# Kernel optimization log

Hardware: AMD Instinct MI355X
Metric: run time of the kernel (lower is better)

## Reference

```python
import jax, jax.numpy as jnp
import numpy as np

# DeformConv hyperparameters (from init_kwargs)
KH, KW = 3, 3
STRIDE, PAD, DIL = 1, 1, 1
GROUPS, DG = 1, 1  # groups=1, deformable_groups=1
B, C, H, W = 4, 64, 128, 128
O = 64
HO = (H + 2 * PAD - (DIL * (KH - 1) + 1)) // STRIDE + 1  # 128
WO = (W + 2 * PAD - (DIL * (KW - 1) + 1)) // STRIDE + 1  # 128


def setup_inputs() -> dict:
    key = jax.random.key(0)
    k1, k2, k3, k4 = jax.random.split(key, 4)
    x = jax.random.normal(k1, (B, C, H, W), dtype=jnp.float32)
    # offset channels: dg * K * 2, ordered (y, x) per kernel tap (DCNv1 CUDA layout)
    offset = jax.random.normal(k2, (B, 2 * DG * KH * KW, HO, WO), dtype=jnp.float32)
    fan_in = C * KH * KW
    weight = jax.random.normal(k3, (O, C // GROUPS, KH, KW), dtype=jnp.float32) / np.sqrt(fan_in)
    bias = jax.random.normal(k4, (O,), dtype=jnp.float32) * 0.01
    return {"x": x, "offset": offset, "weight": weight, "bias": bias}


def _deform_sample(x, offset):
    """Bilinear-sample x at deformed kernel tap locations.
    Returns [B, C, K, HO, WO] where K = KH*KW."""
    K = KH * KW
    Cg = C // DG
    # offset -> [B, DG, K, 2, HO, WO]; channel layout: dg*2*K, pairs (y, x)
    off = offset.reshape(B, DG, K, 2, HO, WO)
    off_y, off_x = off[:, :, :, 0], off[:, :, :, 1]  # [B, DG, K, HO, WO]

    ki = (jnp.arange(K) // KW).astype(jnp.float32)  # kernel row
    kj = (jnp.arange(K) % KW).astype(jnp.float32)   # kernel col
    base_h = (jnp.arange(HO) * STRIDE - PAD).astype(jnp.float32)
    base_w = (jnp.arange(WO) * STRIDE - PAD).astype(jnp.float32)

    # sampling positions [B, DG, K, HO, WO]
    py = off_y + (ki * DIL)[None, None, :, None, None] + base_h[None, None, None, :, None]
    px = off_x + (kj * DIL)[None, None, :, None, None] + base_w[None, None, None, None, :]

    y0f = jnp.floor(py)
    x0f = jnp.floor(px)
    ly = py - y0f
    lx = px - x0f
    hy = 1.0 - ly
    hx = 1.0 - lx
    y0 = y0f.astype(jnp.int32)
    x0 = x0f.astype(jnp.int32)
    y1 = y0 + 1
    x1 = x0 + 1

    flat = x.reshape(B, DG, Cg, H * W)

    def gather(yi, xi, wgt):
        valid = (yi >= 0) & (yi < H) & (xi >= 0) & (xi < W)
        idx = jnp.clip(yi, 0, H - 1) * W + jnp.clip(xi, 0, W - 1)
        idx = idx.reshape(B, DG, 1, K * HO * WO)
        v = jnp.take_along_axis(flat, idx, axis=-1).reshape(B, DG, Cg, K, HO, WO)
        return v * (wgt * valid.astype(wgt.dtype))[:, :, None]

    val = (gather(y0, x0, hy * hx) + gather(y0, x1, hy * lx)
           + gather(y1, x0, ly * hx) + gather(y1, x1, ly * lx))
    return val.reshape(B, C, K, HO, WO)


def reference(x, offset, weight, bias):
    sampled = _deform_sample(x, offset)              # [B, C, K, HO, WO]
    w = weight.reshape(O, C, KH * KW)                # groups = 1
    out = jnp.einsum('bckhw,ock->bohw', sampled, w)  # im2col + GEMM
    return out + bias[None, :, None, None]
```

## Files before the change

### kernel.cpp

```cpp
#include <hip/hip_runtime.h>
#include <hip/hip_fp16.h>


#define B_  4
#define C_  64
#define H_  128
#define W_  128
#define O_  64
#define HO_ 128
#define WO_ 128
#define NCHUNK 8
#define NGW 12
#define NT_ 32
#define NROW 2
#define NCOL 64
#define NTASK (9 * NCOL)
#define SG  10
#define SBUF (SG * NCOL * 8)
#define TR  14
#define TC  44
#define TSLOTS (TR * TC)
#define TBUF (TSLOTS * 8)

typedef _Float16 half8 __attribute__((ext_vector_type(8)));
typedef __attribute__((ext_vector_type(4))) float f32x4;
typedef __attribute__((ext_vector_type(16))) float f32x16;

union H8 { float4 v; __half2 h2[4]; half8 v8; };

__global__ __launch_bounds__(256)
void prep(const float* __restrict__ x, const float* __restrict__ w,
          __half* __restrict__ xt, __half* __restrict__ wt) {
    const int tid = threadIdx.x;
    if (blockIdx.x < 2048) {
        int t = blockIdx.x * 256 + tid;
        int xc = t & 127;
        int y  = (t >> 7) & 127;
        int ch = (t >> 14) & 7;
        int b  = t >> 17;
        const float* xp = x + (((size_t)(b * C_ + ch * 8) * H_) + y) * W_ + xc;
        union { __half h[8]; float4 v; } pk;
#pragma unroll
        for (int e = 0; e < 8; ++e) pk.h[e] = __float2half_rn(xp[e * H_ * W_]);
        *(float4*)(xt + (size_t)t * 8) = pk.v;
    } else {
        int t = (blockIdx.x - 2048) * 256 + tid;
        if (t >= NCHUNK * NGW * O_) return;
        int o  = t & 63;
        int g  = (t >> 6) % NGW;
        int ch = (t >> 6) / NGW;
        union { __half h[8]; float4 v; } pk;
#pragma unroll
        for (int e = 0; e < 8; ++e)
            pk.h[e] = (g < 9) ? __float2half_rn(w[(o * C_ + ch * 8 + e) * 9 + g])
                              : __half(0.0f);
        *(float4*)(wt + (size_t)t * 8) = pk.v;
    }
}

__global__ __launch_bounds__(256, 4)
void dcn_mfma(const __half* __restrict__ xt, const float* __restrict__ off,
              const __half* __restrict__ wt, const float* __restrict__ bias,
              float* __restrict__ out) {
    __shared__ __align__(16) _Float16 sS[2 * SBUF];
    __shared__ __align__(16) _Float16 sT[2 * TBUF];

    const int tid = threadIdx.x;
    const int bid = blockIdx.x;
    const int w4  = bid & 3;
    const int hp  = (bid >> 2) & 63;
    const int b   = bid >> 8;
    const int ho  = hp << 1;
    const int woB = w4 * NT_;
    const int yb  = ho - 6;
    const int xb  = woB - 6;

    int a0_[3], a1_[3], nf_[3];
    __half2 ua2_[3], ub2_[3], va2_[3], vb2_[3];
#pragma unroll
    for (int r = 0; r < 3; ++r) {
        bool act = (r < 2) || ((tid & 3) == 0);
        if (act) {
            int task = (r < 2) ? (tid + r * 256) : (512 + (tid >> 2));
            int k  = task >> 6;
            int n  = task & 63;
            int wo = (n & 31) + woB;
            int hr = ho + (n >> 5);
            int ki = k / 3, kj = k - 3 * ki;
            float oy = off[(((b * 18) + 2 * k    ) * HO_ + hr) * WO_ + wo];
            float ox = off[(((b * 18) + 2 * k + 1) * HO_ + hr) * WO_ + wo];
            float py = (float)(hr - 1 + ki) + oy;
            float px = (float)(wo - 1 + kj) + ox;
            float y0f = floorf(py), x0f = floorf(px);
            int   y0 = (int)y0f,   x0 = (int)x0f;
            float ly = py - y0f,   lx = px - x0f;
            float hy = 1.f - ly,   hx = 1.f - lx;
            int y1 = y0 + 1, x1 = x0 + 1;
            float vy0 = (y0 >= 0 && y0 < H_) ? 1.f : 0.f;
            float vy1 = (y1 >= 0 && y1 < H_) ? 1.f : 0.f;
            float vx0 = (x0 >= 0 && x0 < W_) ? 1.f : 0.f;
            float vx1 = (x1 >= 0 && x1 < W_) ? 1.f : 0.f;
            int cy0 = min(max(y0, 0), H_ - 1), cy1 = min(max(y1, 0), H_ - 1);
            int ax  = min(max(x0, 0), W_ - 2);
            int cx0 = min(max(x0, 0), W_ - 1), cx1 = min(max(x1, 0), W_ - 1);
            float w00 = hy * hx * vy0 * vx0;
            float w01 = hy * lx * vy0 * vx1;
            float w10 = ly * hx * vy1 * vx0;
            float w11 = ly * lx * vy1 * vx1;
            float s0 = (cx0 != ax) ? 1.f : 0.f;
            float s1 = (cx1 != ax) ? 1.f : 0.f;
            int t0 = cy0 - yb, t1 = cy1 - yb, txx = ax - xb;
            int fb = ((unsigned)t0  > (TR - 1)) |
                     ((unsigned)t1  > (TR - 1)) |
                     ((unsigned)txx > (TC - 2));
            nf_[r] = !fb;
            a0_[r] = fb ? (cy0 * W_ + ax) : (t0 * TC + txx);
            a1_[r] = fb ? (cy1 * W_ + ax) : (t1 * TC + txx);
            ua2_[r] = __float2half2_rn(w00 * (1.f - s0) + w01 * (1.f - s1));
            ub2_[r] = __float2half2_rn(w00 * s0 + w01 * s1);
            va2_[r] = __float2half2_rn(w10 * (1.f - s0) + w11 * (1.f - s1));
            vb2_[r] = __float2half2_rn(w10 * s0 + w11 * s1);
        }
    }

    int gofs[3];
#pragma unroll
    for (int j = 0; j < 3; ++j) {
        int s  = tid + j * 256;
        int sc = (s < TSLOTS) ? s : (TSLOTS - 1);
        int rr = sc / TC, cc = sc - rr * TC;
        int yc = min(max(yb + rr, 0), H_ - 1);
        int xc = min(max(xb + cc, 0), W_ - 1);
        gofs[j] = yc * W_ + xc;
    }

    ((unsigned int*)&sS[9 * NCOL * 8])[tid]        = 0u;
    ((unsigned int*)&sS[SBUF + 9 * NCOL * 8])[tid] = 0u;

    float4 pf0, pf1, pf2;
    auto issue = [&](int ch) {
        const float4* xc = (const float4*)(xt + ((size_t)(b * NCHUNK + ch)) * (H_ * W_ * 8));
        pf0 = xc[gofs[0]];
        pf1 = xc[gofs[1]];
        if (tid < TSLOTS - 512) pf2 = xc[gofs[2]];
    };
    auto tile_write = [&](int parity) {
        float4* tw = (float4*)(sT + parity * TBUF);
        tw[tid]       = pf0;
        tw[tid + 256] = pf1;
        if (tid < TSLOTS - 512) tw[tid + 512] = pf2;
    };

    auto sample = [&](int ch) {
        _Float16* buf = sS + (ch & 1) * SBUF;
        const float4* xcg = (const float4*)(xt + ((size_t)(b * NCHUNK + ch)) * (H_ * W_ * 8));
        const float4* tl  = (const float4*)(sT + (ch & 1) * TBUF);
#pragma unroll
        for (int r = 0; r < 3; ++r) {
            bool act = (r < 2) || ((tid & 3) == 0);
            if (act) {
                int task = (r < 2) ? (tid + r * 256) : (512 + (tid >> 2));
                int k = task >> 6;
                int n = task & 63;
                int a0 = a0_[r], a1 = a1_[r];
                H8 q00, q01, q10, q11;
                if (nf_[r]) {
                    q00.v = tl[a0];  q01.v = tl[a0 + 1];
                    q10.v = tl[a1];  q11.v = tl[a1 + 1];
                } else {
                    q00.v = xcg[a0]; q01.v = xcg[a0 + 1];
                    q10.v = xcg[a1]; q11.v = xcg[a1 + 1];
                }
                H8 s;
#pragma unroll
                for (int j = 0; j < 4; ++j) {
                    __half2 t0 = __hmul2(ua2_[r], q00.h2[j]);
                    t0 = __hfma2(ub2_[r], q01.h2[j], t0);
                    t0 = __hfma2(va2_[r], q10.h2[j], t0);
                    t0 = __hfma2(vb2_[r], q11.h2[j], t0);
                    s.h2[j] = t0;
                }
                *(half8*)&buf[(k * NCOL + n) * 8] = s.v8;
            }
        }
    };

    const int lane = tid & 63;
    const int wv   = tid >> 6;
    const int ow   = wv & 1;
    const int nw   = wv >> 1;
    const int h2k  = lane >> 5;
    const int l31  = lane & 31;

    f32x16 acc = {0.f, 0.f, 0.f, 0.f, 0.f, 0.f, 0.f, 0.f,
                  0.f, 0.f, 0.f, 0.f, 0.f, 0.f, 0.f, 0.f};

    auto mfma_chunk = [&](int ch) {
        const __half*   wc  = wt + (size_t)(ch * NGW) * O_ * 8;
        const _Float16* buf = sS + (ch & 1) * SBUF;
#pragma unroll
        for (int ks = 0; ks < 6; ++ks) {
            int g  = 2 * ks + h2k;
            int gb = (g < 9) ? g : 9;
            half8 bfr = *(const half8*)&buf[(gb * NCOL + nw * 32 + l31) * 8];
            half8 afr = *(const half8*)(wc + (size_t)(g * O_ + ow * 32 + l31) * 8);
            acc = __builtin_amdgcn_mfma_f32_32x32x16_f16(afr, bfr, acc, 0, 0, 0);
        }
    };

    issue(0);
    tile_write(0);
    for (int ch = 0; ch < NCHUNK; ++ch) {
        __syncthreads();
        if (ch + 1 < NCHUNK) issue(ch + 1);
        sample(ch);
        if (ch > 0) mfma_chunk(ch - 1);
        if (ch + 1 < NCHUNK) tile_write((ch + 1) & 1);
    }
    __syncthreads();
    mfma_chunk(NCHUNK - 1);

    {
        int wo = woB + l31;
        size_t base = (((size_t)b * O_) * HO_ + ho + nw) * WO_ + wo;
#pragma unroll
        for (int rg = 0; rg < 16; ++rg) {
            int o = ow * 32 + (rg & 3) + 8 * (rg >> 2) + 4 * h2k;
            out[base + (size_t)o * HO_ * WO_] = acc[rg] + bias[o];
        }
    }
}

extern "C" void kernel_launch(void* const* d_in, const int* in_sizes, int n_in,
                              void* d_out, int out_size, void* d_ws, size_t ws_size,
                              hipStream_t stream) {
    const float* x    = (const float*)d_in[0];
    const float* off  = (const float*)d_in[1];
    const float* w    = (const float*)d_in[2];
    const float* bias = (const float*)d_in[3];
    float* out = (float*)d_out;

    __half* wt = (__half*)d_ws;
    __half* xt = (__half*)((char*)d_ws + 262144);

    hipLaunchKernelGGL(prep, dim3(2048 + 24), dim3(256), 0, stream, x, w, xt, wt);
    hipLaunchKernelGGL(dcn_mfma, dim3(B_ * (HO_ / NROW) * (WO_ / NT_)), dim3(256), 0, stream,
                       xt, off, wt, bias, out);
}
```

Before: 98.41 us.

## Fuse x fp16 transpose into DCN kernel, read NCHW fp32 directly

Removes the separate pass that converted x into a channel-interleaved fp16 buffer. The main kernel now loads fp32 x from NCHW, eight scalar loads per slot, and converts to half when staging the shared tile and in the out-of-tile fallback path. The third task round moves from every fourth thread to the last wave, so the extra work sits in one wavefront instead of causing divergence in all of them. This saves a full read and write of x plus one launch, but each tile load now issues strided scalar reads with more registers held, and the fallback gathers become much more expensive.

```diff
diff --git a/kernel.cpp b/kernel.cpp
--- a/kernel.cpp
+++ b/kernel.cpp
@@ -21,6 +21,7 @@
 #define TC  44
 #define TSLOTS (TR * TC)
 #define TBUF (TSLOTS * 8)
+#define HW_ (H_ * W_)
 
 typedef _Float16 half8 __attribute__((ext_vector_type(8)));
 typedef __attribute__((ext_vector_type(4))) float f32x4;
@@ -29,37 +30,22 @@
 union H8 { float4 v; __half2 h2[4]; half8 v8; };
 
 __global__ __launch_bounds__(256)
-void prep(const float* __restrict__ x, const float* __restrict__ w,
-          __half* __restrict__ xt, __half* __restrict__ wt) {
-    const int tid = threadIdx.x;
-    if (blockIdx.x < 2048) {
-        int t = blockIdx.x * 256 + tid;
-        int xc = t & 127;
-        int y  = (t >> 7) & 127;
-        int ch = (t >> 14) & 7;
-        int b  = t >> 17;
-        const float* xp = x + (((size_t)(b * C_ + ch * 8) * H_) + y) * W_ + xc;
-        union { __half h[8]; float4 v; } pk;
-#pragma unroll
-        for (int e = 0; e < 8; ++e) pk.h[e] = __float2half_rn(xp[e * H_ * W_]);
-        *(float4*)(xt + (size_t)t * 8) = pk.v;
-    } else {
-        int t = (blockIdx.x - 2048) * 256 + tid;
-        if (t >= NCHUNK * NGW * O_) return;
-        int o  = t & 63;
-        int g  = (t >> 6) % NGW;
-        int ch = (t >> 6) / NGW;
-        union { __half h[8]; float4 v; } pk;
-#pragma unroll
-        for (int e = 0; e < 8; ++e)
-            pk.h[e] = (g < 9) ? __float2half_rn(w[(o * C_ + ch * 8 + e) * 9 + g])
-                              : __half(0.0f);
-        *(float4*)(wt + (size_t)t * 8) = pk.v;
-    }
+void prep_wt(const float* __restrict__ w, __half* __restrict__ wt) {
+    int t = blockIdx.x * 256 + threadIdx.x;
+    if (t >= NCHUNK * NGW * O_) return;
+    int o  = t & 63;
+    int g  = (t >> 6) % NGW;
+    int ch = (t >> 6) / NGW;
+    union { __half h[8]; float4 v; } pk;
+#pragma unroll
+    for (int e = 0; e < 8; ++e)
+        pk.h[e] = (g < 9) ? __float2half_rn(w[(o * C_ + ch * 8 + e) * 9 + g])
+                          : __half(0.0f);
+    *(float4*)(wt + (size_t)t * 8) = pk.v;
 }
 
 __global__ __launch_bounds__(256, 4)
-void dcn_mfma(const __half* __restrict__ xt, const float* __restrict__ off,
+void dcn_mfma(const float* __restrict__ x, const float* __restrict__ off,
               const __half* __restrict__ wt, const float* __restrict__ bias,
               float* __restrict__ out) {
     __shared__ __align__(16) _Float16 sS[2 * SBUF];
@@ -75,13 +61,15 @@
     const int yb  = ho - 6;
     const int xb  = woB - 6;
 
+    const float* xb_ = x + (size_t)b * C_ * HW_;
+
     int a0_[3], a1_[3], nf_[3];
     __half2 ua2_[3], ub2_[3], va2_[3], vb2_[3];
 #pragma unroll
     for (int r = 0; r < 3; ++r) {
-        bool act = (r < 2) || ((tid & 3) == 0);
+        bool act = (r < 2) || (tid >= 192);
         if (act) {
-            int task = (r < 2) ? (tid + r * 256) : (512 + (tid >> 2));
+            int task = (r < 2) ? (tid + r * 256) : (512 + (tid & 63));
             int k  = task >> 6;
             int n  = task & 63;
             int wo = (n & 31) + woB;
@@ -137,29 +125,41 @@
     ((unsigned int*)&sS[9 * NCOL * 8])[tid]        = 0u;
     ((unsigned int*)&sS[SBUF + 9 * NCOL * 8])[tid] = 0u;
 
-    float4 pf0, pf1, pf2;
+    float pfv[3][8];
     auto issue = [&](int ch) {
-        const float4* xc = (const float4*)(xt + ((size_t)(b * NCHUNK + ch)) * (H_ * W_ * 8));
-        pf0 = xc[gofs[0]];
-        pf1 = xc[gofs[1]];
-        if (tid < TSLOTS - 512) pf2 = xc[gofs[2]];
+        const float* xc = xb_ + (size_t)(ch * 8) * HW_;
+#pragma unroll
+        for (int j = 0; j < 3; ++j) {
+            if (j < 2 || tid < TSLOTS - 512) {
+#pragma unroll
+                for (int e = 0; e < 8; ++e)
+                    pfv[j][e] = xc[(size_t)e * HW_ + gofs[j]];
+            }
+        }
     };
     auto tile_write = [&](int parity) {
         float4* tw = (float4*)(sT + parity * TBUF);
-        tw[tid]       = pf0;
-        tw[tid + 256] = pf1;
-        if (tid < TSLOTS - 512) tw[tid + 512] = pf2;
+#pragma unroll
+        for (int j = 0; j < 3; ++j) {
+            if (j < 2 || tid < TSLOTS - 512) {
+                H8 pk;
+#pragma unroll
+                for (int jj = 0; jj < 4; ++jj)
+                    pk.h2[jj] = __floats2half2_rn(pfv[j][2 * jj], pfv[j][2 * jj + 1]);
+                tw[tid + j * 256] = pk.v;
+            }
+        }
     };
 
     auto sample = [&](int ch) {
         _Float16* buf = sS + (ch & 1) * SBUF;
-        const float4* xcg = (const float4*)(xt + ((size_t)(b * NCHUNK + ch)) * (H_ * W_ * 8));
-        const float4* tl  = (const float4*)(sT + (ch & 1) * TBUF);
+        const float* xcg = xb_ + (size_t)(ch * 8) * HW_;
+        const float4* tl = (const float4*)(sT + (ch & 1) * TBUF);
 #pragma unroll
         for (int r = 0; r < 3; ++r) {
-            bool act = (r < 2) || ((tid & 3) == 0);
+            bool act = (r < 2) || (tid >= 192);
             if (act) {
-                int task = (r < 2) ? (tid + r * 256) : (512 + (tid >> 2));
+                int task = (r < 2) ? (tid + r * 256) : (512 + (tid & 63));
                 int k = task >> 6;
                 int n = task & 63;
                 int a0 = a0_[r], a1 = a1_[r];
@@ -168,8 +168,18 @@
                     q00.v = tl[a0];  q01.v = tl[a0 + 1];
                     q10.v = tl[a1];  q11.v = tl[a1 + 1];
                 } else {
-                    q00.v = xcg[a0]; q01.v = xcg[a0 + 1];
-                    q10.v = xcg[a1]; q11.v = xcg[a1 + 1];
+#pragma unroll
+                    for (int jj = 0; jj < 4; ++jj) {
+                        int e0 = 2 * jj, e1 = 2 * jj + 1;
+                        q00.h2[jj] = __floats2half2_rn(xcg[(size_t)e0 * HW_ + a0],
+                                                       xcg[(size_t)e1 * HW_ + a0]);
+                        q01.h2[jj] = __floats2half2_rn(xcg[(size_t)e0 * HW_ + a0 + 1],
+                                                       xcg[(size_t)e1 * HW_ + a0 + 1]);
+                        q10.h2[jj] = __floats2half2_rn(xcg[(size_t)e0 * HW_ + a1],
+                                                       xcg[(size_t)e1 * HW_ + a1]);
+                        q11.h2[jj] = __floats2half2_rn(xcg[(size_t)e0 * HW_ + a1 + 1],
+                                                       xcg[(size_t)e1 * HW_ + a1 + 1]);
+                    }
                 }
                 H8 s;
 #pragma unroll
@@ -241,9 +251,8 @@
     float* out = (float*)d_out;
 
     __half* wt = (__half*)d_ws;
-    __half* xt = (__half*)((char*)d_ws + 262144);
-
-    hipLaunchKernelGGL(prep, dim3(2048 + 24), dim3(256), 0, stream, x, w, xt, wt);
+
+    hipLaunchKernelGGL(prep_wt, dim3(24), dim3(256), 0, stream, w, wt);
     hipLaunchKernelGGL(dcn_mfma, dim3(B_ * (HO_ / NROW) * (WO_ / NT_)), dim3(256), 0, stream,
-                       xt, off, wt, bias, out);
+                       x, off, wt, bias, out);
 }
```

Result: slower. 106.1 us (+7.8%).

## Feed bilinear samples directly into 16x16x32 MFMA registers, dropping shared staging

Applied to the files above, without the earlier changes.

Sampled values are no longer written to a shared-memory im2col buffer and read back for a 32x32 MFMA. Each wave now computes its own sampled B-fragment in registers and feeds it straight into four 16x16x32 MFMAs, one per 16-output tile. The halo tile grows to 16x48 so the slot count matches the 768 threads' loads exactly, which removes the predicated load. This drops the LDS round trip and the separate sample/MFMA pipeline stage. In exchange, weight fragments are reloaded per wave, the pipeline depth shrinks, and some lanes do dummy work for the padded taps.

```diff
diff --git a/kernel.cpp b/kernel.cpp
--- a/kernel.cpp
+++ b/kernel.cpp
@@ -13,18 +13,14 @@
 #define NGW 12
 #define NT_ 32
 #define NROW 2
-#define NCOL 64
-#define NTASK (9 * NCOL)
-#define SG  10
-#define SBUF (SG * NCOL * 8)
-#define TR  14
-#define TC  44
+#define TR  16
+#define TC  48
 #define TSLOTS (TR * TC)
 #define TBUF (TSLOTS * 8)
+#define HW_ (H_ * W_)
 
 typedef _Float16 half8 __attribute__((ext_vector_type(8)));
 typedef __attribute__((ext_vector_type(4))) float f32x4;
-typedef __attribute__((ext_vector_type(16))) float f32x16;
 
 union H8 { float4 v; __half2 h2[4]; half8 v8; };
 
@@ -62,7 +58,6 @@
 void dcn_mfma(const __half* __restrict__ xt, const float* __restrict__ off,
               const __half* __restrict__ wt, const float* __restrict__ bias,
               float* __restrict__ out) {
-    __shared__ __align__(16) _Float16 sS[2 * SBUF];
     __shared__ __align__(16) _Float16 sT[2 * TBUF];
 
     const int tid = threadIdx.x;
@@ -73,22 +68,25 @@
     const int ho  = hp << 1;
     const int woB = w4 * NT_;
     const int yb  = ho - 6;
-    const int xb  = woB - 6;
+    const int xb  = woB - 8;
+
+    const int lane = tid & 63;
+    const int wv   = tid >> 6;
+    const int quad = lane >> 4;
+    const int l15  = lane & 15;
+    const int n    = wv * 16 + l15;
+    const int hr   = ho + (n >> 5);
+    const int wo   = woB + (n & 31);
 
     int a0_[3], a1_[3], nf_[3];
     __half2 ua2_[3], ub2_[3], va2_[3], vb2_[3];
 #pragma unroll
-    for (int r = 0; r < 3; ++r) {
-        bool act = (r < 2) || ((tid & 3) == 0);
-        if (act) {
-            int task = (r < 2) ? (tid + r * 256) : (512 + (tid >> 2));
-            int k  = task >> 6;
-            int n  = task & 63;
-            int wo = (n & 31) + woB;
-            int hr = ho + (n >> 5);
-            int ki = k / 3, kj = k - 3 * ki;
-            float oy = off[(((b * 18) + 2 * k    ) * HO_ + hr) * WO_ + wo];
-            float ox = off[(((b * 18) + 2 * k + 1) * HO_ + hr) * WO_ + wo];
+    for (int ks = 0; ks < 3; ++ks) {
+        int g = ks * 4 + quad;
+        if (g < 9) {
+            int ki = g / 3, kj = g - 3 * ki;
+            float oy = off[(((b * 18) + 2 * g    ) * HO_ + hr) * WO_ + wo];
+            float ox = off[(((b * 18) + 2 * g + 1) * HO_ + hr) * WO_ + wo];
             float py = (float)(hr - 1 + ki) + oy;
             float px = (float)(wo - 1 + kj) + ox;
             float y0f = floorf(py), x0f = floorf(px);
@@ -113,13 +111,16 @@
             int fb = ((unsigned)t0  > (TR - 1)) |
                      ((unsigned)t1  > (TR - 1)) |
                      ((unsigned)txx > (TC - 2));
-            nf_[r] = !fb;
-            a0_[r] = fb ? (cy0 * W_ + ax) : (t0 * TC + txx);
-            a1_[r] = fb ? (cy1 * W_ + ax) : (t1 * TC + txx);
-            ua2_[r] = __float2half2_rn(w00 * (1.f - s0) + w01 * (1.f - s1));
-            ub2_[r] = __float2half2_rn(w00 * s0 + w01 * s1);
-            va2_[r] = __float2half2_rn(w10 * (1.f - s0) + w11 * (1.f - s1));
-            vb2_[r] = __float2half2_rn(w10 * s0 + w11 * s1);
+            nf_[ks] = !fb;
+            a0_[ks] = fb ? (cy0 * W_ + ax) : (t0 * TC + txx);
+            a1_[ks] = fb ? (cy1 * W_ + ax) : (t1 * TC + txx);
+            ua2_[ks] = __float2half2_rn(w00 * (1.f - s0) + w01 * (1.f - s1));
+            ub2_[ks] = __float2half2_rn(w00 * s0 + w01 * s1);
+            va2_[ks] = __float2half2_rn(w10 * (1.f - s0) + w11 * (1.f - s1));
+            vb2_[ks] = __float2half2_rn(w10 * s0 + w11 * s1);
+        } else {
+            nf_[ks] = 1; a0_[ks] = 0; a1_[ks] = 0;
+            ua2_[ks] = ub2_[ks] = va2_[ks] = vb2_[ks] = __float2half2_rn(0.f);
         }
     }
 
@@ -127,84 +128,61 @@
 #pragma unroll
     for (int j = 0; j < 3; ++j) {
         int s  = tid + j * 256;
-        int sc = (s < TSLOTS) ? s : (TSLOTS - 1);
-        int rr = sc / TC, cc = sc - rr * TC;
+        int rr = s / TC, cc = s - rr * TC;
         int yc = min(max(yb + rr, 0), H_ - 1);
         int xc = min(max(xb + cc, 0), W_ - 1);
         gofs[j] = yc * W_ + xc;
     }
 
-    ((unsigned int*)&sS[9 * NCOL * 8])[tid]        = 0u;
-    ((unsigned int*)&sS[SBUF + 9 * NCOL * 8])[tid] = 0u;
-
     float4 pf0, pf1, pf2;
     auto issue = [&](int ch) {
-        const float4* xc = (const float4*)(xt + ((size_t)(b * NCHUNK + ch)) * (H_ * W_ * 8));
+        const float4* xc = (const float4*)(xt + ((size_t)(b * NCHUNK + ch)) * (HW_ * 8));
         pf0 = xc[gofs[0]];
         pf1 = xc[gofs[1]];
-        if (tid < TSLOTS - 512) pf2 = xc[gofs[2]];
+        pf2 = xc[gofs[2]];
     };
     auto tile_write = [&](int parity) {
         float4* tw = (float4*)(sT + parity * TBUF);
         tw[tid]       = pf0;
         tw[tid + 256] = pf1;
-        if (tid < TSLOTS - 512) tw[tid + 512] = pf2;
+        tw[tid + 512] = pf2;
     };
 
-    auto sample = [&](int ch) {
-        _Float16* buf = sS + (ch & 1) * SBUF;
-        const float4* xcg = (const float4*)(xt + ((size_t)(b * NCHUNK + ch)) * (H_ * W_ * 8));
+    f32x4 acc[4];
+#pragma unroll
+    for (int ot = 0; ot < 4; ++ot) acc[ot] = (f32x4){0.f, 0.f, 0.f, 0.f};
+
+    auto compute = [&](int ch) {
         const float4* tl  = (const float4*)(sT + (ch & 1) * TBUF);
-#pragma unroll
-        for (int r = 0; r < 3; ++r) {
-            bool act = (r < 2) || ((tid & 3) == 0);
-            if (act) {
-                int task = (r < 2) ? (tid + r * 256) : (512 + (tid >> 2));
-                int k = task >> 6;
-                int n = task & 63;
-                int a0 = a0_[r], a1 = a1_[r];
-                H8 q00, q01, q10, q11;
-                if (nf_[r]) {
-                    q00.v = tl[a0];  q01.v = tl[a0 + 1];
-                    q10.v = tl[a1];  q11.v = tl[a1 + 1];
-                } else {
-                    q00.v = xcg[a0]; q01.v = xcg[a0 + 1];
-                    q10.v = xcg[a1]; q11.v = xcg[a1 + 1];
-                }
-                H8 s;
-#pragma unroll
-                for (int j = 0; j < 4; ++j) {
-                    __half2 t0 = __hmul2(ua2_[r], q00.h2[j]);
-                    t0 = __hfma2(ub2_[r], q01.h2[j], t0);
-                    t0 = __hfma2(va2_[r], q10.h2[j], t0);
-                    t0 = __hfma2(vb2_[r], q11.h2[j], t0);
-                    s.h2[j] = t0;
-                }
-                *(half8*)&buf[(k * NCOL + n) * 8] = s.v8;
-            }
-        }
-    };
-
-    const int lane = tid & 63;
-    const int wv   = tid >> 6;
-    const int ow   = wv & 1;
-    const int nw   = wv >> 1;
-    const int h2k  = lane >> 5;
-    const int l31  = lane & 31;
-
-    f32x16 acc = {0.f, 0.f, 0.f, 0.f, 0.f, 0.f, 0.f, 0.f,
-                  0.f, 0.f, 0.f, 0.f, 0.f, 0.f, 0.f, 0.f};
-
-    auto mfma_chunk = [&](int ch) {
-        const __half*   wc  = wt + (size_t)(ch * NGW) * O_ * 8;
-        const _Float16* buf = sS + (ch & 1) * SBUF;
-#pragma unroll
-        for (int ks = 0; ks < 6; ++ks) {
-            int g  = 2 * ks + h2k;
-            int gb = (g < 9) ? g : 9;
-            half8 bfr = *(const half8*)&buf[(gb * NCOL + nw * 32 + l31) * 8];
-            half8 afr = *(const half8*)(wc + (size_t)(g * O_ + ow * 32 + l31) * 8);
-            acc = __builtin_amdgcn_mfma_f32_32x32x16_f16(afr, bfr, acc, 0, 0, 0);
+        const float4* xcg = (const float4*)(xt + ((size_t)(b * NCHUNK + ch)) * (HW_ * 8));
+        const __half* wc  = wt + (size_t)(ch * NGW) * O_ * 8;
+#pragma unroll
+        for (int ks = 0; ks < 3; ++ks) {
+            int g = ks * 4 + quad;
+            H8 q00, q01, q10, q11;
+            if (nf_[ks]) {
+                int a0 = a0_[ks], a1 = a1_[ks];
+                q00.v = tl[a0];  q01.v = tl[a0 + 1];
+                q10.v = tl[a1];  q11.v = tl[a1 + 1];
+            } else {
+                int a0 = a0_[ks], a1 = a1_[ks];
+                q00.v = xcg[a0]; q01.v = xcg[a0 + 1];
+                q10.v = xcg[a1]; q11.v = xcg[a1 + 1];
+            }
+            H8 s;
+#pragma unroll
+            for (int j = 0; j < 4; ++j) {
+                __half2 t0 = __hmul2(ua2_[ks], q00.h2[j]);
+                t0 = __hfma2(ub2_[ks], q01.h2[j], t0);
+                t0 = __hfma2(va2_[ks], q10.h2[j], t0);
+                t0 = __hfma2(vb2_[ks], q11.h2[j], t0);
+                s.h2[j] = t0;
+            }
+#pragma unroll
+            for (int ot = 0; ot < 4; ++ot) {
+                half8 afr = *(const half8*)(wc + (size_t)(g * O_ + ot * 16 + l15) * 8);
+                acc[ot] = __builtin_amdgcn_mfma_f32_16x16x32_f16(afr, s.v8, acc[ot], 0, 0, 0);
+            }
         }
     };
 
@@ -213,21 +191,21 @@
     for (int ch = 0; ch < NCHUNK; ++ch) {
         __syncthreads();
         if (ch + 1 < NCHUNK) issue(ch + 1);
-        sample(ch);
-        if (ch > 0) mfma_chunk(ch - 1);
+        compute(ch);
         if (ch + 1 < NCHUNK) tile_write((ch + 1) & 1);
     }
-    __syncthreads();
-    mfma_chunk(NCHUNK - 1);
 
     {
-        int wo = woB + l31;
-        size_t base = (((size_t)b * O_) * HO_ + ho + nw) * WO_ + wo;
-#pragma unroll
-        for (int rg = 0; rg < 16; ++rg) {
-            int o = ow * 32 + (rg & 3) + 8 * (rg >> 2) + 4 * h2k;
-            out[base + (size_t)o * HO_ * WO_] = acc[rg] + bias[o];
-        }
+        int row = wv >> 1;
+        int woo = woB + (wv & 1) * 16 + l15;
+        size_t base = (((size_t)(b * O_)) * HO_ + ho + row) * WO_ + woo;
+#pragma unroll
+        for (int ot = 0; ot < 4; ++ot)
+#pragma unroll
+            for (int rg = 0; rg < 4; ++rg) {
+                int o = ot * 16 + quad * 4 + rg;
+                out[base + (size_t)o * HO_ * WO_] = acc[ot][rg] + bias[o];
+            }
     }
 }
 
```

Measured after the change: 98.42 us. Within noise of the previous version (+0.0%).
